# Performance work log

Measured on AMD Instinct MI355X. Metric: run time of the kernel, lower is better.

Reference implementation:

```python
import jax, jax.numpy as jnp
import numpy as np

B, L, HID, NH = 1, 2048, 3072, 24
HD = HID // NH          # 128
MLP = HID * 4           # 12288


def _layernorm(x, eps=1e-6):
    # LayerNorm without affine (pre_norm)
    mu = jnp.mean(x, axis=-1, keepdims=True)
    var = jnp.mean(jnp.square(x - mu), axis=-1, keepdims=True)
    return (x - mu) * jax.lax.rsqrt(var + eps)


def _rmsnorm(x, w):
    # torch.nn.RMSNorm with eps=None -> finfo(dtype).eps
    eps = jnp.finfo(x.dtype).eps
    ms = jnp.mean(jnp.square(x), axis=-1, keepdims=True)
    return x * jax.lax.rsqrt(ms + eps) * w


def _apply_rope(x, pe):
    # x: (B, L, H, D); pe: (B, 1, L, D//2, 2, 2)
    b, l, h, d = x.shape
    x_ = x.astype(jnp.float32).reshape(b, l, h, d // 2, 1, 2)
    f = pe[:, :, :, None]                       # (B,1,L,1,D//2,2,2)
    out = f[..., 0] * x_[..., 0] + f[..., 1] * x_[..., 1]
    return out.reshape(b, l, h, d).astype(x.dtype)


def setup_inputs() -> dict:
    key = jax.random.key(0)
    ks = jax.random.split(key, 16)
    s = 0.02
    # pe as proper 2x2 rotation matrices (EmbedND output structure)
    theta = jax.random.uniform(ks[0], (L, HD // 2), minval=0.0, maxval=2.0 * np.pi)
    cos, sin = jnp.cos(theta), jnp.sin(theta)
    rot = jnp.stack([jnp.stack([cos, -sin], -1), jnp.stack([sin, cos], -1)], -2)
    pe = rot[None, None].astype(jnp.float32)    # (1,1,L,HD//2,2,2)
    rnd = lambda k, shp: jax.random.normal(k, shp, jnp.float32)
    return {
        "x": rnd(ks[1], (B, L, HID)),
        "vec": rnd(ks[2], (B, HID)),
        "pe": pe,
        "w_mod": rnd(ks[3], (HID, 3 * HID)) * s,
        "b_mod": rnd(ks[4], (3 * HID,)) * s,
        "w_qkv": rnd(ks[5], (HID, 3 * HID)) * s,
        "b_qkv": rnd(ks[6], (3 * HID,)) * s,
        "w_fc1": rnd(ks[7], (HID, MLP)) * s,
        "b_fc1": rnd(ks[8], (MLP,)) * s,
        "w_fc2": rnd(ks[9], (MLP, HID)) * s,
        "b_fc2": rnd(ks[10], (HID,)) * s,
        "w_out": rnd(ks[11], (HID, HID)) * s,
        "b_out": rnd(ks[12], (HID,)) * s,
        "norm_q_w": jnp.ones((HD,), jnp.float32),
        "norm_k_w": jnp.ones((HD,), jnp.float32),
    }


def reference(x, vec, pe, w_mod, b_mod, w_qkv, b_qkv, w_fc1, b_fc1,
              w_fc2, b_fc2, w_out, b_out, norm_q_w, norm_k_w):
    # modulation: AWQ linear on silu(vec)
    mod = jax.nn.silu(vec) @ w_mod + b_mod            # (B, 3*HID)
    shift, scale, gate = jnp.split(mod[:, None, :], 3, axis=-1)
    x_mod = _layernorm(x) * (1.0 + scale) + shift      # (B, L, HID)

    # qkv projection (SVDQ linear, dequantized math == dense GEMM)
    qkv = x_mod @ w_qkv + b_qkv
    q, k, v = jnp.split(qkv, 3, axis=-1)
    q = _rmsnorm(q.reshape(B, L, NH, HD), norm_q_w)
    k = _rmsnorm(k.reshape(B, L, NH, HD), norm_k_w)
    q = _apply_rope(q, pe)
    k = _apply_rope(k, pe)
    v = v.reshape(B, L, NH, HD)

    # scaled dot-product attention
    scores = jnp.einsum("blhd,bmhd->bhlm", q, k) / jnp.sqrt(jnp.float32(HD))
    probs = jax.nn.softmax(scores, axis=-1)
    attn = jnp.einsum("bhlm,bmhd->blhd", probs, v).reshape(B, L, HID)

    # parallel MLP branch
    mlp = jax.nn.gelu(x_mod @ w_fc1 + b_fc1, approximate=True)
    mlp = mlp @ w_fc2 + b_fc2

    out = attn @ w_out + b_out + mlp
    return x + gate * out
```

## Files before the change

### kernel.cpp

```cpp
#include <hip/hip_runtime.h>
#include <hip/hip_bf16.h>
#include <stdint.h>


typedef __bf16 bf16;
typedef bf16 bf16x2 __attribute__((ext_vector_type(2)));
typedef bf16 bf16x4 __attribute__((ext_vector_type(4)));
typedef bf16 bf16x8 __attribute__((ext_vector_type(8)));
typedef float f32x4 __attribute__((ext_vector_type(4)));

#define L_SEQ 2048
#define HIDD  3072
#define NHH   24
#define HDD   128
#define MLPD  12288
#define N3Q   9216

__device__ __forceinline__ void gload_lds16(const bf16* g, bf16* l) {
  __builtin_amdgcn_global_load_lds(
      (const __attribute__((address_space(1))) unsigned int*)g,
      (__attribute__((address_space(3))) unsigned int*)l, 16, 0, 0);
}

__device__ __forceinline__ float gelu_tanh(float x) {
  float z = 0.7978845608028654f * (x + 0.044715f * x * x * x);
  float t = 1.f - 2.f / (__expf(2.f * z) + 1.f);
  return 0.5f * x * (1.f + t);
}

__global__ __launch_bounds__(256) void mod_partial(
    const float* __restrict__ vec, const float* __restrict__ w_mod,
    float* __restrict__ part) {
  __shared__ float sv[256];
  int y = blockIdx.y;
  int i0 = y * 256;
  {
    float xv = vec[i0 + threadIdx.x];
    sv[threadIdx.x] = xv / (1.f + __expf(-xv));
  }
  __syncthreads();
  int j = blockIdx.x * 256 + threadIdx.x;
  float acc = 0.f;
#pragma unroll 8
  for (int i = 0; i < 256; ++i)
    acc += sv[i] * w_mod[(size_t)(i0 + i) * N3Q + j];
  part[y * N3Q + j] = acc;
}

__global__ __launch_bounds__(256) void mod_reduce(
    const float* __restrict__ part, const float* __restrict__ b_mod,
    float* __restrict__ mod) {
  int j = blockIdx.x * 256 + threadIdx.x;
  float s = b_mod[j];
#pragma unroll
  for (int p = 0; p < 12; ++p) s += part[p * N3Q + j];
  mod[j] = s;
}

__global__ __launch_bounds__(256) void ln_mod_k(
    const float* __restrict__ x, const float* __restrict__ mod,
    bf16* __restrict__ xm) {
  __shared__ float sb[4];
  int l = blockIdx.x, t = threadIdx.x;
  const float* xr = x + (size_t)l * HIDD;
  float4 v[3];
  float s = 0.f;
#pragma unroll
  for (int p = 0; p < 3; ++p) {
    v[p] = *(const float4*)(xr + p * 1024 + t * 4);
    s += v[p].x + v[p].y + v[p].z + v[p].w;
  }
#pragma unroll
  for (int o = 32; o >= 1; o >>= 1) s += __shfl_xor(s, o);
  if (!(t & 63)) sb[t >> 6] = s;
  __syncthreads();
  float mean = (sb[0] + sb[1] + sb[2] + sb[3]) * (1.f / HIDD);
  __syncthreads();
  float vs = 0.f;
#pragma unroll
  for (int p = 0; p < 3; ++p) {
    float a = v[p].x - mean, b = v[p].y - mean, c = v[p].z - mean,
          d = v[p].w - mean;
    vs += a * a + b * b + c * c + d * d;
  }
#pragma unroll
  for (int o = 32; o >= 1; o >>= 1) vs += __shfl_xor(vs, o);
  if (!(t & 63)) sb[t >> 6] = vs;
  __syncthreads();
  float var = (sb[0] + sb[1] + sb[2] + sb[3]) * (1.f / HIDD);
  float rs = rsqrtf(var + 1e-6f);
#pragma unroll
  for (int p = 0; p < 3; ++p) {
    int j = p * 1024 + t * 4;
    float4 sc = *(const float4*)(mod + HIDD + j);
    float4 sh = *(const float4*)(mod + j);
    bf16x4 o;
    o[0] = (bf16)((v[p].x - mean) * rs * (1.f + sc.x) + sh.x);
    o[1] = (bf16)((v[p].y - mean) * rs * (1.f + sc.y) + sh.y);
    o[2] = (bf16)((v[p].z - mean) * rs * (1.f + sc.z) + sh.z);
    o[3] = (bf16)((v[p].w - mean) * rs * (1.f + sc.w) + sh.w);
    *(bf16x4*)(xm + (size_t)l * HIDD + j) = o;
  }
}

__global__ __launch_bounds__(256) void convT(
    const float* __restrict__ src, bf16* __restrict__ dst, int K, int N) {
  __shared__ bf16 tl[64 * 72];
  int n0 = blockIdx.x * 64, k0 = blockIdx.y * 64;
  int t = threadIdx.x;
#pragma unroll
  for (int p = 0; p < 4; ++p) {
    int idx = p * 256 + t;
    int kr = idx >> 4, c4 = (idx & 15) << 2;
    float4 v = *(const float4*)(src + (size_t)(k0 + kr) * N + n0 + c4);
    bf16x4 b;
    b[0] = (bf16)v.x; b[1] = (bf16)v.y; b[2] = (bf16)v.z; b[3] = (bf16)v.w;
    *(bf16x4*)(tl + kr * 72 + c4) = b;
  }
  __syncthreads();
#pragma unroll
  for (int p = 0; p < 2; ++p) {
    int idx = p * 256 + t;
    int nr = idx >> 3, c = idx & 7;
    bf16x8 o;
#pragma unroll
    for (int j = 0; j < 8; ++j) o[j] = tl[(c * 8 + j) * 72 + nr];
    *(bf16x8*)(dst + (size_t)(n0 + nr) * K + k0 + c * 8) = o;
  }
}

template <int EPI>
__global__ __launch_bounds__(256) void gemm_bt(
    const bf16* __restrict__ A, const bf16* __restrict__ BT,
    const float* __restrict__ bias, int lda, int klen,
    float* __restrict__ e_p0, float* __restrict__ e_p1,
    bf16* __restrict__ o0, bf16* __restrict__ o1, bf16* __restrict__ o2) {
  __shared__ bf16 As[2][128 * 64];
  __shared__ bf16 Bs[2][128 * 64];
  const int tid = threadIdx.x;
  const int lane = tid & 63, w = tid >> 6;
  const int wm = w >> 1, wn = w & 1;
  const int g = lane >> 4, r16 = lane & 15;
  const int row0 = blockIdx.x * 128, col0 = blockIdx.y * 128;
  const int kb = (EPI == 4) ? blockIdx.z * klen : 0;

  const int s_rr = tid >> 3, s_cc = tid & 7;
  const bf16* gA = A + (size_t)(row0 + s_rr) * lda + kb + ((s_cc ^ (s_rr & 7)) << 3);
  const bf16* gB = BT + (size_t)(col0 + s_rr) * lda + kb + ((s_cc ^ (s_rr & 7)) << 3);

  f32x4 acc[4][4] = {};

#define STAGE(buf, koff)                                                      \
  {                                                                           \
    _Pragma("unroll") for (int p = 0; p < 4; ++p) {                           \
      gload_lds16(gA + (size_t)(p * 32) * lda + (koff),                       \
                  &As[buf][(p * 4 + w) << 9]);                                \
      gload_lds16(gB + (size_t)(p * 32) * lda + (koff),                       \
                  &Bs[buf][(p * 4 + w) << 9]);                                \
    }                                                                         \
  }

  const int nk = klen >> 6;
  STAGE(0, 0);
  asm volatile("s_waitcnt vmcnt(0)" ::: "memory");
  __builtin_amdgcn_s_barrier();
  __builtin_amdgcn_sched_barrier(0);

  int cur = 0;
  for (int it = 0; it < nk; ++it) {
    if (it + 1 < nk) STAGE(cur ^ 1, (it + 1) * 64);
    const bf16* as = As[cur];
    const bf16* bs = Bs[cur];
#pragma unroll
    for (int kk = 0; kk < 2; ++kk) {
      bf16x8 af[4], bff[4];
#pragma unroll
      for (int m = 0; m < 4; ++m) {
        int rr = wm * 64 + m * 16 + r16;
        af[m] = *(const bf16x8*)(as + rr * 64 + (((kk * 4 + g) ^ (rr & 7)) << 3));
      }
#pragma unroll
      for (int n = 0; n < 4; ++n) {
        int rr = wn * 64 + n * 16 + r16;
        bff[n] = *(const bf16x8*)(bs + rr * 64 + (((kk * 4 + g) ^ (rr & 7)) << 3));
      }
#pragma unroll
      for (int m = 0; m < 4; ++m)
#pragma unroll
        for (int n = 0; n < 4; ++n)
          acc[m][n] = __builtin_amdgcn_mfma_f32_16x16x32_bf16(
              af[m], bff[n], acc[m][n], 0, 0, 0);
    }
    __builtin_amdgcn_sched_barrier(0);
    asm volatile("s_waitcnt vmcnt(0)" ::: "memory");
    __builtin_amdgcn_s_barrier();
    __builtin_amdgcn_sched_barrier(0);
    cur ^= 1;
  }
#undef STAGE

  float* psel = (EPI == 4) ? (blockIdx.z ? e_p1 : e_p0) : e_p0;
#pragma unroll
  for (int m = 0; m < 4; ++m) {
    int row = row0 + wm * 64 + m * 16 + g * 4;
#pragma unroll
    for (int n = 0; n < 4; ++n) {
      int col = col0 + wn * 64 + n * 16 + r16;
      float bv = (EPI == 4) ? 0.f : bias[col];
#pragma unroll
      for (int r = 0; r < 4; ++r) {
        float v = acc[m][n][r] + bv;
        if (EPI == 0) {
          bf16* dst;
          int cl = col;
          if (col < 3072) { dst = o0; }
          else if (col < 6144) { dst = o1; cl -= 3072; }
          else { dst = o2; cl -= 6144; }
          dst[(size_t)(row + r) * HIDD + cl] = (bf16)v;
        } else if (EPI == 1) {
          o0[(size_t)(row + r) * MLPD + col] = (bf16)gelu_tanh(v);
        } else {
          psel[(size_t)(row + r) * HIDD + col] = v;
        }
      }
    }
  }
}

__global__ __launch_bounds__(256) void final_k(
    const float* __restrict__ x, const float* __restrict__ tmp,
    const float* __restrict__ p0, const float* __restrict__ p1,
    const float* __restrict__ mod, const float* __restrict__ b_fc2,
    float* __restrict__ out) {
  int l = blockIdx.x, t = threadIdx.x;
#pragma unroll
  for (int p = 0; p < 3; ++p) {
    int c = p * 1024 + t * 4;
    size_t idx = (size_t)l * HIDD + c;
    float4 xv = *(const float4*)(x + idx);
    float4 tv = *(const float4*)(tmp + idx);
    float4 a0 = *(const float4*)(p0 + idx);
    float4 a1 = *(const float4*)(p1 + idx);
    float4 gv = *(const float4*)(mod + 2 * HIDD + c);
    float4 bv = *(const float4*)(b_fc2 + c);
    float4 o;
    o.x = xv.x + gv.x * (tv.x + a0.x + a1.x + bv.x);
    o.y = xv.y + gv.y * (tv.y + a0.y + a1.y + bv.y);
    o.z = xv.z + gv.z * (tv.z + a0.z + a1.z + bv.z);
    o.w = xv.w + gv.w * (tv.w + a0.w + a1.w + bv.w);
    *(float4*)(out + idx) = o;
  }
}

__global__ __launch_bounds__(256) void qknorm_rope_k(
    bf16* __restrict__ q, bf16* __restrict__ k, const float* __restrict__ pe,
    const float* __restrict__ qw, const float* __restrict__ kw) {
  int t = threadIdx.x, lane = t & 63, w = t >> 6;
  int pair = blockIdx.x * 4 + w;
  int h = pair % NHH, l = pair / NHH;
  size_t base = (size_t)l * HIDD + h * HDD + 2 * lane;
  float4 f = *(const float4*)(pe + (size_t)l * 256 + lane * 4);
  float2 wq = *(const float2*)(qw + 2 * lane);
  float2 wk = *(const float2*)(kw + 2 * lane);
  {
    bf16x2 xv = *(bf16x2*)(q + base);
    float x0 = (float)xv[0], x1 = (float)xv[1];
    float ss = x0 * x0 + x1 * x1;
#pragma unroll
    for (int o = 32; o >= 1; o >>= 1) ss += __shfl_xor(ss, o);
    float rs = rsqrtf(ss * (1.f / HDD) + 1.1920929e-7f);
    x0 *= rs * wq.x; x1 *= rs * wq.y;
    const float qs = 0.08838834764831845f;
    bf16x2 ov;
    ov[0] = (bf16)((f.x * x0 + f.y * x1) * qs);
    ov[1] = (bf16)((f.z * x0 + f.w * x1) * qs);
    *(bf16x2*)(q + base) = ov;
  }
  {
    bf16x2 xv = *(bf16x2*)(k + base);
    float x0 = (float)xv[0], x1 = (float)xv[1];
    float ss = x0 * x0 + x1 * x1;
#pragma unroll
    for (int o = 32; o >= 1; o >>= 1) ss += __shfl_xor(ss, o);
    float rs = rsqrtf(ss * (1.f / HDD) + 1.1920929e-7f);
    x0 *= rs * wk.x; x1 *= rs * wk.y;
    bf16x2 ov;
    ov[0] = (bf16)(f.x * x0 + f.y * x1);
    ov[1] = (bf16)(f.z * x0 + f.w * x1);
    *(bf16x2*)(k + base) = ov;
  }
}

__global__ __launch_bounds__(256) void vtrans_k(
    const bf16* __restrict__ v, bf16* __restrict__ vt) {
  __shared__ bf16 tl[128 * 128];
  int t = threadIdx.x, lt = blockIdx.x, h = blockIdx.y;
#pragma unroll
  for (int p = 0; p < 8; ++p) {
    int idx = p * 256 + t;
    int i = idx >> 4, c = idx & 15;
    bf16x8 val =
        *(const bf16x8*)(v + (size_t)(lt * 128 + i) * HIDD + h * HDD + c * 8);
    *(bf16x8*)(tl + i * 128 + ((c ^ (i & 15)) << 3)) = val;
  }
  __syncthreads();
#pragma unroll
  for (int p = 0; p < 8; ++p) {
    int idx = p * 256 + t;
    int j = idx >> 4, i8 = (idx & 15) << 3;
    bf16x8 o;
#pragma unroll
    for (int e = 0; e < 8; ++e) {
      int row = i8 + e;
      o[e] = tl[row * 128 + ((((j >> 3) ^ (row & 15)) << 3) | (j & 7))];
    }
    *(bf16x8*)(vt + ((size_t)h * HDD + j) * L_SEQ + lt * 128 + i8) = o;
  }
}

__global__ __launch_bounds__(256) void attn_k(
    const bf16* __restrict__ q, const bf16* __restrict__ k,
    const bf16* __restrict__ vt, bf16* __restrict__ out) {
  __shared__ bf16 Ks[64 * 128];
  __shared__ bf16 Vs[128 * 64];
  __shared__ bf16 Ps[4][16 * 72];
  int tid = threadIdx.x, lane = tid & 63, w = tid >> 6;
  int g = lane >> 4, r16 = lane & 15;
  int qt = blockIdx.x, h = blockIdx.y;
  int qbase = qt * 64 + w * 16;

  bf16x8 qreg[4];
  const bf16* qrow = q + (size_t)(qbase + r16) * HIDD + h * HDD;
#pragma unroll
  for (int c = 0; c < 4; ++c) qreg[c] = *(const bf16x8*)(qrow + c * 32 + g * 8);

  f32x4 acc[8] = {};
  float m_run = -3.0e38f, l_run = 0.f;
  bf16* ps = &Ps[w][0];

  for (int kv0 = 0; kv0 < L_SEQ; kv0 += 64) {
    __syncthreads();
#pragma unroll
    for (int p = 0; p < 4; ++p) {
      int ci = p * 256 + tid;
      {
        int rr = ci >> 4, cc = ci & 15;
        gload_lds16(k + (size_t)(kv0 + rr) * HIDD + h * HDD +
                        ((cc ^ (rr & 15)) << 3),
                    Ks + ((p * 4 + w) << 9));
      }
      {
        int rr = ci >> 3, cc = ci & 7;
        gload_lds16(vt + ((size_t)h * HDD + rr) * L_SEQ + kv0 +
                        ((cc ^ (rr & 7)) << 3),
                    Vs + ((p * 4 + w) << 9));
      }
    }
    __syncthreads();

    f32x4 st[4] = {};
#pragma unroll
    for (int m4 = 0; m4 < 4; ++m4) {
#pragma unroll
      for (int c = 0; c < 4; ++c) {
        int rr = m4 * 16 + r16;
        bf16x8 kf =
            *(const bf16x8*)(Ks + rr * 128 + (((c * 4 + g) ^ (rr & 15)) << 3));
        st[m4] =
            __builtin_amdgcn_mfma_f32_16x16x32_bf16(kf, qreg[c], st[m4], 0, 0, 0);
      }
    }
    float cmax = -3.0e38f;
#pragma unroll
    for (int m4 = 0; m4 < 4; ++m4)
#pragma unroll
      for (int r = 0; r < 4; ++r) cmax = fmaxf(cmax, st[m4][r]);
    cmax = fmaxf(cmax, __shfl_xor(cmax, 16));
    cmax = fmaxf(cmax, __shfl_xor(cmax, 32));
    float m_new = fmaxf(m_run, cmax);
    float corr = __expf(m_run - m_new);
    float psum = 0.f;
#pragma unroll
    for (int m4 = 0; m4 < 4; ++m4) {
      bf16x4 pk;
#pragma unroll
      for (int r = 0; r < 4; ++r) {
        float pv = __expf(st[m4][r] - m_new);
        psum += pv;
        pk[r] = (bf16)pv;
      }
      *(bf16x4*)(ps + r16 * 72 + m4 * 16 + g * 4) = pk;
    }
    psum += __shfl_xor(psum, 16);
    psum += __shfl_xor(psum, 32);
    l_run = l_run * corr + psum;
    m_run = m_new;
    float corr_r[4];
#pragma unroll
    for (int r = 0; r < 4; ++r) corr_r[r] = __shfl(corr, g * 4 + r);
#pragma unroll
    for (int nt = 0; nt < 8; ++nt)
#pragma unroll
      for (int r = 0; r < 4; ++r) acc[nt][r] *= corr_r[r];
#pragma unroll
    for (int ks = 0; ks < 2; ++ks) {
      bf16x8 pf = *(const bf16x8*)(ps + r16 * 72 + ks * 32 + g * 8);
#pragma unroll
      for (int nt = 0; nt < 8; ++nt) {
        int rr = nt * 16 + r16;
        bf16x8 vf =
            *(const bf16x8*)(Vs + rr * 64 + (((ks * 4 + g) ^ (rr & 7)) << 3));
        acc[nt] = __builtin_amdgcn_mfma_f32_16x16x32_bf16(pf, vf, acc[nt], 0, 0, 0);
      }
    }
  }
  float inv = 1.f / l_run;
  float inv_r[4];
#pragma unroll
  for (int r = 0; r < 4; ++r) inv_r[r] = __shfl(inv, g * 4 + r);
#pragma unroll
  for (int nt = 0; nt < 8; ++nt)
#pragma unroll
    for (int r = 0; r < 4; ++r)
      out[(size_t)(qbase + g * 4 + r) * HIDD + h * HDD + nt * 16 + r16] =
          (bf16)(acc[nt][r] * inv_r[r]);
}

extern "C" void kernel_launch(void* const* d_in, const int* in_sizes, int n_in,
                              void* d_out, int out_size, void* d_ws,
                              size_t ws_size, hipStream_t stream) {
  const float* x     = (const float*)d_in[0];
  const float* vec   = (const float*)d_in[1];
  const float* pe    = (const float*)d_in[2];
  const float* w_mod = (const float*)d_in[3];
  const float* b_mod = (const float*)d_in[4];
  const float* w_qkv = (const float*)d_in[5];
  const float* b_qkv = (const float*)d_in[6];
  const float* w_fc1 = (const float*)d_in[7];
  const float* b_fc1 = (const float*)d_in[8];
  const float* w_fc2 = (const float*)d_in[9];
  const float* b_fc2 = (const float*)d_in[10];
  const float* w_out = (const float*)d_in[11];
  const float* b_out = (const float*)d_in[12];
  const float* qw    = (const float*)d_in[13];
  const float* kw    = (const float*)d_in[14];
  float* out = (float*)d_out;

  char* ws = (char*)d_ws;
  float* mod  = (float*)(ws + 0);
  bf16* xmod  = (bf16*)(ws + 36864);
  bf16* qb    = (bf16*)(ws + 12619776);
  bf16* kb    = (bf16*)(ws + 25202688);
  bf16* vb    = (bf16*)(ws + 37785600);
  bf16* vt    = (bf16*)(ws + 50368512);
  bf16* att   = (bf16*)(ws + 62951424);
  bf16* mlp   = (bf16*)(ws + 75534336);
  float* tmp  = (float*)(ws + 125865984);
  bf16* wt    = (bf16*)(ws + 151031808);
  float* part = (float*)(ws + 125865984);
  float* pC   = (float*)(ws + 12619776);
  float* pD   = (float*)(ws + 37785600);

  mod_partial<<<dim3(36, 12), 256, 0, stream>>>(vec, w_mod, part);
  mod_reduce<<<36, 256, 0, stream>>>(part, b_mod, mod);
  ln_mod_k<<<2048, 256, 0, stream>>>(x, mod, xmod);

  convT<<<dim3(144, 48), 256, 0, stream>>>(w_qkv, wt, 3072, 9216);
  gemm_bt<0><<<dim3(16, 72), 256, 0, stream>>>(xmod, wt, b_qkv, 3072, 3072,
                                               nullptr, nullptr, qb, kb, vb);

  qknorm_rope_k<<<12288, 256, 0, stream>>>(qb, kb, pe, qw, kw);
  vtrans_k<<<dim3(16, 24), 256, 0, stream>>>(vb, vt);
  attn_k<<<dim3(32, 24), 256, 0, stream>>>(qb, kb, vt, att);

  convT<<<dim3(48, 48), 256, 0, stream>>>(w_out, wt, 3072, 3072);
  gemm_bt<2><<<dim3(16, 24), 256, 0, stream>>>(att, wt, b_out, 3072, 3072,
                                               tmp, nullptr, nullptr, nullptr,
                                               nullptr);

  convT<<<dim3(192, 48), 256, 0, stream>>>(w_fc1, wt, 3072, 12288);
  gemm_bt<1><<<dim3(16, 96), 256, 0, stream>>>(xmod, wt, b_fc1, 3072, 3072,
                                               nullptr, nullptr, mlp, nullptr,
                                               nullptr);

  convT<<<dim3(48, 192), 256, 0, stream>>>(w_fc2, wt, 12288, 3072);
  gemm_bt<4><<<dim3(16, 24, 2), 256, 0, stream>>>(mlp, wt, nullptr, 12288,
                                                  6144, pC, pD, nullptr,
                                                  nullptr, nullptr);
  final_k<<<2048, 256, 0, stream>>>(x, tmp, pC, pD, mod, b_fc2, out);
}
```

Baseline: 925.4 us.

## Replace 128x128 GEMM with 256x256 8-wave pipelined GEMM and split-K bf16 partials

```diff
diff --git a/kernel.cpp b/kernel.cpp
--- a/kernel.cpp
+++ b/kernel.cpp
@@ -15,6 +15,8 @@
 #define HDD   128
 #define MLPD  12288
 #define N3Q   9216
+
+struct PB { bf16* p[8]; };
 
 __device__ __forceinline__ void gload_lds16(const bf16* g, bf16* l) {
   __builtin_amdgcn_global_load_lds(
@@ -130,141 +132,154 @@
 }
 
 template <int EPI>
-__global__ __launch_bounds__(256) void gemm_bt(
+__global__ __launch_bounds__(512, 2) void gemm256(
     const bf16* __restrict__ A, const bf16* __restrict__ BT,
-    const float* __restrict__ bias, int lda, int klen,
-    float* __restrict__ e_p0, float* __restrict__ e_p1,
-    bf16* __restrict__ o0, bf16* __restrict__ o1, bf16* __restrict__ o2) {
-  __shared__ bf16 As[2][128 * 64];
-  __shared__ bf16 Bs[2][128 * 64];
+    const float* __restrict__ bias, int lda, int klen, int ldc, PB dst,
+    bf16* __restrict__ o1) {
+  __shared__ bf16 LA[2][2][8192];
+  __shared__ bf16 LB[2][2][8192];
   const int tid = threadIdx.x;
-  const int lane = tid & 63, w = tid >> 6;
-  const int wm = w >> 1, wn = w & 1;
+  const int w = tid >> 6, lane = tid & 63;
+  const int wm = w >> 2, wn = w & 3;
   const int g = lane >> 4, r16 = lane & 15;
-  const int row0 = blockIdx.x * 128, col0 = blockIdx.y * 128;
-  const int kb = (EPI == 4) ? blockIdx.z * klen : 0;
-
-  const int s_rr = tid >> 3, s_cc = tid & 7;
-  const bf16* gA = A + (size_t)(row0 + s_rr) * lda + kb + ((s_cc ^ (s_rr & 7)) << 3);
-  const bf16* gB = BT + (size_t)(col0 + s_rr) * lda + kb + ((s_cc ^ (s_rr & 7)) << 3);
-
-  f32x4 acc[4][4] = {};
-
-#define STAGE(buf, koff)                                                      \
-  {                                                                           \
-    _Pragma("unroll") for (int p = 0; p < 4; ++p) {                           \
-      gload_lds16(gA + (size_t)(p * 32) * lda + (koff),                       \
-                  &As[buf][(p * 4 + w) << 9]);                                \
-      gload_lds16(gB + (size_t)(p * 32) * lda + (koff),                       \
-                  &Bs[buf][(p * 4 + w) << 9]);                                \
-    }                                                                         \
-  }
-
+  const int row0 = blockIdx.x * 256, col0 = blockIdx.y * 256;
+  const size_t kb = (size_t)blockIdx.z * klen;
+
+  const int s_r = tid >> 3, s_c = tid & 7;
+  const bf16* gA = A + (size_t)(row0 + s_r) * lda + kb + ((s_c ^ (s_r & 7)) << 3);
+  const bf16* gB = BT + (size_t)(col0 + s_r) * lda + kb + ((s_c ^ (s_r & 7)) << 3);
+  const int wofs = w * 512;
+
+#define STG_A(buf, h, t)                                                       \
+  do {                                                                         \
+    gload_lds16(gA + (size_t)((h) * 128) * lda + (t) * 64, &LA[buf][h][wofs]); \
+    gload_lds16(gA + (size_t)((h) * 128 + 64) * lda + (t) * 64,                \
+                &LA[buf][h][4096 + wofs]);                                     \
+  } while (0)
+#define STG_B(buf, h, t)                                                       \
+  do {                                                                         \
+    gload_lds16(gB + (size_t)((h) * 128) * lda + (t) * 64, &LB[buf][h][wofs]); \
+    gload_lds16(gB + (size_t)((h) * 128 + 64) * lda + (t) * 64,                \
+                &LB[buf][h][4096 + wofs]);                                     \
+  } while (0)
+#define LGKM0()                                               \
+  do {                                                        \
+    asm volatile("s_waitcnt lgkmcnt(0)" ::: "memory");        \
+    __builtin_amdgcn_sched_barrier(0);                        \
+  } while (0)
+#define MF(mb, AF, BF)                                                     \
+  do {                                                                     \
+    __builtin_amdgcn_s_setprio(1);                                         \
+    _Pragma("unroll") for (int m_ = 0; m_ < 4; ++m_)                       \
+        _Pragma("unroll") for (int n_ = 0; n_ < 4; ++n_)                   \
+            acc[(mb) + m_][n_] = __builtin_amdgcn_mfma_f32_16x16x32_bf16(  \
+                AF[(mb) + m_], BF[n_], acc[(mb) + m_][n_], 0, 0, 0);       \
+    __builtin_amdgcn_s_setprio(0);                                         \
+  } while (0)
+
+  f32x4 acc[8][4] = {};
   const int nk = klen >> 6;
-  STAGE(0, 0);
-  asm volatile("s_waitcnt vmcnt(0)" ::: "memory");
+  const int swz0 = (g ^ (r16 & 7)) << 3;
+  const int swz1 = ((4 + g) ^ (r16 & 7)) << 3;
+  const int brow = (wn & 1) * 64;
+  const int hb = wn >> 1;
+
+  STG_A(0, 0, 0); STG_A(0, 1, 0); STG_B(0, 0, 0); STG_B(0, 1, 0);
+  STG_B(1, 0, 1); STG_A(1, 0, 1); STG_A(1, 1, 1);
+  asm volatile("s_waitcnt vmcnt(6)" ::: "memory");
   __builtin_amdgcn_s_barrier();
-  __builtin_amdgcn_sched_barrier(0);
-
-  int cur = 0;
-  for (int it = 0; it < nk; ++it) {
-    if (it + 1 < nk) STAGE(cur ^ 1, (it + 1) * 64);
-    const bf16* as = As[cur];
-    const bf16* bs = Bs[cur];
-#pragma unroll
-    for (int kk = 0; kk < 2; ++kk) {
-      bf16x8 af[4], bff[4];
-#pragma unroll
-      for (int m = 0; m < 4; ++m) {
-        int rr = wm * 64 + m * 16 + r16;
-        af[m] = *(const bf16x8*)(as + rr * 64 + (((kk * 4 + g) ^ (rr & 7)) << 3));
-      }
-#pragma unroll
-      for (int n = 0; n < 4; ++n) {
-        int rr = wn * 64 + n * 16 + r16;
-        bff[n] = *(const bf16x8*)(bs + rr * 64 + (((kk * 4 + g) ^ (rr & 7)) << 3));
-      }
-#pragma unroll
-      for (int m = 0; m < 4; ++m)
-#pragma unroll
-        for (int n = 0; n < 4; ++n)
-          acc[m][n] = __builtin_amdgcn_mfma_f32_16x16x32_bf16(
-              af[m], bff[n], acc[m][n], 0, 0, 0);
-    }
-    __builtin_amdgcn_sched_barrier(0);
-    asm volatile("s_waitcnt vmcnt(0)" ::: "memory");
-    __builtin_amdgcn_s_barrier();
-    __builtin_amdgcn_sched_barrier(0);
-    cur ^= 1;
-  }
-#undef STAGE
-
-  float* psel = (EPI == 4) ? (blockIdx.z ? e_p1 : e_p0) : e_p0;
-#pragma unroll
-  for (int m = 0; m < 4; ++m) {
-    int row = row0 + wm * 64 + m * 16 + g * 4;
+
+  for (int t = 0; t < nk; ++t) {
+    const int buf = t & 1;
+    const bf16* la = LA[buf][wm];
+    const bf16* lb = LB[buf][hb];
+    bf16x8 af0[8], af1[8], bf0[4], bf1[4];
+
+#pragma unroll
+    for (int m = 0; m < 8; ++m)
+      af0[m] = *(const bf16x8*)(la + (m * 16 + r16) * 64 + swz0);
+#pragma unroll
+    for (int n = 0; n < 4; ++n)
+      bf0[n] = *(const bf16x8*)(lb + (brow + n * 16 + r16) * 64 + swz0);
+    __builtin_amdgcn_s_barrier();
+    LGKM0();
+    if (t + 1 < nk) STG_B(buf ^ 1, 1, t + 1);
+    MF(0, af0, bf0);
+    __builtin_amdgcn_s_barrier();
+
+#pragma unroll
+    for (int n = 0; n < 4; ++n)
+      bf1[n] = *(const bf16x8*)(lb + (brow + n * 16 + r16) * 64 + swz1);
+    __builtin_amdgcn_s_barrier();
+    LGKM0();
+    if (t + 2 < nk) STG_B(buf, 0, t + 2);
+    MF(4, af0, bf0);
+    __builtin_amdgcn_s_barrier();
+
+#pragma unroll
+    for (int m = 0; m < 4; ++m)
+      af1[m] = *(const bf16x8*)(la + (m * 16 + r16) * 64 + swz1);
+    __builtin_amdgcn_s_barrier();
+    LGKM0();
+    MF(0, af1, bf1);
+    __builtin_amdgcn_s_barrier();
+
+#pragma unroll
+    for (int m = 4; m < 8; ++m)
+      af1[m] = *(const bf16x8*)(la + (m * 16 + r16) * 64 + swz1);
+    __builtin_amdgcn_s_barrier();
+    LGKM0();
+    if (t + 2 < nk) { STG_A(buf, 0, t + 2); STG_A(buf, 1, t + 2); }
+    if (t < nk - 2) {
+      asm volatile("s_waitcnt vmcnt(6)" ::: "memory");
+    } else if (t == nk - 2) {
+      asm volatile("s_waitcnt vmcnt(0)" ::: "memory");
+    }
+    MF(4, af1, bf1);
+    __builtin_amdgcn_s_barrier();
+  }
+#undef STG_A
+#undef STG_B
+#undef LGKM0
+#undef MF
+
+  bf16* dp = (EPI == 0) ? dst.p[blockIdx.z] : o1;
+#pragma unroll
+  for (int m = 0; m < 8; ++m) {
+    int row = row0 + wm * 128 + m * 16 + g * 4;
 #pragma unroll
     for (int n = 0; n < 4; ++n) {
       int col = col0 + wn * 64 + n * 16 + r16;
-      float bv = (EPI == 4) ? 0.f : bias[col];
+      float bv = (EPI == 1) ? bias[col] : 0.f;
 #pragma unroll
       for (int r = 0; r < 4; ++r) {
         float v = acc[m][n][r] + bv;
-        if (EPI == 0) {
-          bf16* dst;
-          int cl = col;
-          if (col < 3072) { dst = o0; }
-          else if (col < 6144) { dst = o1; cl -= 3072; }
-          else { dst = o2; cl -= 6144; }
-          dst[(size_t)(row + r) * HIDD + cl] = (bf16)v;
-        } else if (EPI == 1) {
-          o0[(size_t)(row + r) * MLPD + col] = (bf16)gelu_tanh(v);
-        } else {
-          psel[(size_t)(row + r) * HIDD + col] = v;
-        }
+        if (EPI == 1) v = gelu_tanh(v);
+        dp[(size_t)(row + r) * ldc + col] = (bf16)v;
       }
     }
   }
 }
 
-__global__ __launch_bounds__(256) void final_k(
-    const float* __restrict__ x, const float* __restrict__ tmp,
-    const float* __restrict__ p0, const float* __restrict__ p1,
-    const float* __restrict__ mod, const float* __restrict__ b_fc2,
-    float* __restrict__ out) {
-  int l = blockIdx.x, t = threadIdx.x;
-#pragma unroll
-  for (int p = 0; p < 3; ++p) {
-    int c = p * 1024 + t * 4;
-    size_t idx = (size_t)l * HIDD + c;
-    float4 xv = *(const float4*)(x + idx);
-    float4 tv = *(const float4*)(tmp + idx);
-    float4 a0 = *(const float4*)(p0 + idx);
-    float4 a1 = *(const float4*)(p1 + idx);
-    float4 gv = *(const float4*)(mod + 2 * HIDD + c);
-    float4 bv = *(const float4*)(b_fc2 + c);
-    float4 o;
-    o.x = xv.x + gv.x * (tv.x + a0.x + a1.x + bv.x);
-    o.y = xv.y + gv.y * (tv.y + a0.y + a1.y + bv.y);
-    o.z = xv.z + gv.z * (tv.z + a0.z + a1.z + bv.z);
-    o.w = xv.w + gv.w * (tv.w + a0.w + a1.w + bv.w);
-    *(float4*)(out + idx) = o;
-  }
-}
-
 __global__ __launch_bounds__(256) void qknorm_rope_k(
-    bf16* __restrict__ q, bf16* __restrict__ k, const float* __restrict__ pe,
-    const float* __restrict__ qw, const float* __restrict__ kw) {
+    const bf16* __restrict__ P0, const bf16* __restrict__ P1,
+    const float* __restrict__ b_qkv, const float* __restrict__ pe,
+    const float* __restrict__ qw, const float* __restrict__ kw,
+    bf16* __restrict__ qb, bf16* __restrict__ kb) {
   int t = threadIdx.x, lane = t & 63, w = t >> 6;
   int pair = blockIdx.x * 4 + w;
   int h = pair % NHH, l = pair / NHH;
-  size_t base = (size_t)l * HIDD + h * HDD + 2 * lane;
+  size_t qi = (size_t)l * N3Q + h * HDD + 2 * lane;
+  size_t ob = (size_t)l * HIDD + h * HDD + 2 * lane;
   float4 f = *(const float4*)(pe + (size_t)l * 256 + lane * 4);
   float2 wq = *(const float2*)(qw + 2 * lane);
   float2 wk = *(const float2*)(kw + 2 * lane);
   {
-    bf16x2 xv = *(bf16x2*)(q + base);
-    float x0 = (float)xv[0], x1 = (float)xv[1];
+    bf16x2 a = *(const bf16x2*)(P0 + qi);
+    bf16x2 b = *(const bf16x2*)(P1 + qi);
+    float2 bq = *(const float2*)(b_qkv + h * HDD + 2 * lane);
+    float x0 = (float)a[0] + (float)b[0] + bq.x;
+    float x1 = (float)a[1] + (float)b[1] + bq.y;
     float ss = x0 * x0 + x1 * x1;
 #pragma unroll
     for (int o = 32; o >= 1; o >>= 1) ss += __shfl_xor(ss, o);
@@ -274,11 +289,14 @@
     bf16x2 ov;
     ov[0] = (bf16)((f.x * x0 + f.y * x1) * qs);
     ov[1] = (bf16)((f.z * x0 + f.w * x1) * qs);
-    *(bf16x2*)(q + base) = ov;
+    *(bf16x2*)(qb + ob) = ov;
   }
   {
-    bf16x2 xv = *(bf16x2*)(k + base);
-    float x0 = (float)xv[0], x1 = (float)xv[1];
+    bf16x2 a = *(const bf16x2*)(P0 + qi + HIDD);
+    bf16x2 b = *(const bf16x2*)(P1 + qi + HIDD);
+    float2 bk = *(const float2*)(b_qkv + HIDD + h * HDD + 2 * lane);
+    float x0 = (float)a[0] + (float)b[0] + bk.x;
+    float x1 = (float)a[1] + (float)b[1] + bk.y;
     float ss = x0 * x0 + x1 * x1;
 #pragma unroll
     for (int o = 32; o >= 1; o >>= 1) ss += __shfl_xor(ss, o);
@@ -287,20 +305,27 @@
     bf16x2 ov;
     ov[0] = (bf16)(f.x * x0 + f.y * x1);
     ov[1] = (bf16)(f.z * x0 + f.w * x1);
-    *(bf16x2*)(k + base) = ov;
+    *(bf16x2*)(kb + ob) = ov;
   }
 }
 
 __global__ __launch_bounds__(256) void vtrans_k(
-    const bf16* __restrict__ v, bf16* __restrict__ vt) {
+    const bf16* __restrict__ P0, const bf16* __restrict__ P1,
+    const float* __restrict__ b_qkv, bf16* __restrict__ vt) {
   __shared__ bf16 tl[128 * 128];
   int t = threadIdx.x, lt = blockIdx.x, h = blockIdx.y;
 #pragma unroll
   for (int p = 0; p < 8; ++p) {
     int idx = p * 256 + t;
     int i = idx >> 4, c = idx & 15;
-    bf16x8 val =
-        *(const bf16x8*)(v + (size_t)(lt * 128 + i) * HIDD + h * HDD + c * 8);
+    size_t gi = (size_t)(lt * 128 + i) * N3Q + 2 * HIDD + h * HDD + c * 8;
+    bf16x8 a = *(const bf16x8*)(P0 + gi);
+    bf16x8 b = *(const bf16x8*)(P1 + gi);
+    bf16x8 val;
+#pragma unroll
+    for (int e = 0; e < 8; ++e)
+      val[e] = (bf16)((float)a[e] + (float)b[e] +
+                      b_qkv[2 * HIDD + h * HDD + c * 8 + e]);
     *(bf16x8*)(tl + i * 128 + ((c ^ (i & 15)) << 3)) = val;
   }
   __syncthreads();
@@ -424,6 +449,51 @@
     for (int r = 0; r < 4; ++r)
       out[(size_t)(qbase + g * 4 + r) * HIDD + h * HDD + nt * 16 + r16] =
           (bf16)(acc[nt][r] * inv_r[r]);
+}
+
+__global__ __launch_bounds__(256) void osum_k(
+    const bf16* __restrict__ a, const bf16* __restrict__ b,
+    float* __restrict__ o) {
+  size_t i = ((size_t)blockIdx.x * 256 + threadIdx.x) * 4;
+  bf16x4 va = *(const bf16x4*)(a + i);
+  bf16x4 vb = *(const bf16x4*)(b + i);
+  float4 s;
+  s.x = (float)va[0] + (float)vb[0];
+  s.y = (float)va[1] + (float)vb[1];
+  s.z = (float)va[2] + (float)vb[2];
+  s.w = (float)va[3] + (float)vb[3];
+  *(float4*)(o + i) = s;
+}
+
+__global__ __launch_bounds__(256) void final_k(
+    const float* __restrict__ x, PB ps, const float* __restrict__ mod,
+    const float* __restrict__ b_out, const float* __restrict__ b_fc2,
+    float* __restrict__ out) {
+  int l = blockIdx.x, t = threadIdx.x;
+#pragma unroll
+  for (int p = 0; p < 3; ++p) {
+    int c = p * 1024 + t * 4;
+    size_t idx = (size_t)l * HIDD + c;
+    float4 xv = *(const float4*)(x + idx);
+    float4 gv = *(const float4*)(mod + 2 * HIDD + c);
+    float4 bo = *(const float4*)(b_out + c);
+    float4 bf = *(const float4*)(b_fc2 + c);
+    float4 da = *(const float4*)(out + idx);
+    float a0 = da.x + bo.x + bf.x, a1 = da.y + bo.y + bf.y;
+    float a2 = da.z + bo.z + bf.z, a3 = da.w + bo.w + bf.w;
+#pragma unroll
+    for (int i = 0; i < 8; ++i) {
+      bf16x4 v = *(const bf16x4*)(ps.p[i] + idx);
+      a0 += (float)v[0]; a1 += (float)v[1];
+      a2 += (float)v[2]; a3 += (float)v[3];
+    }
+    float4 o;
+    o.x = xv.x + gv.x * a0;
+    o.y = xv.y + gv.y * a1;
+    o.z = xv.z + gv.z * a2;
+    o.w = xv.w + gv.w * a3;
+    *(float4*)(out + idx) = o;
+  }
 }
 
 extern "C" void kernel_launch(void* const* d_in, const int* in_sizes, int n_in,
@@ -450,42 +520,54 @@
   float* mod  = (float*)(ws + 0);
   bf16* xmod  = (bf16*)(ws + 36864);
   bf16* qb    = (bf16*)(ws + 12619776);
-  bf16* kb    = (bf16*)(ws + 25202688);
-  bf16* vb    = (bf16*)(ws + 37785600);
-  bf16* vt    = (bf16*)(ws + 50368512);
-  bf16* att   = (bf16*)(ws + 62951424);
-  bf16* mlp   = (bf16*)(ws + 75534336);
-  float* tmp  = (float*)(ws + 125865984);
-  bf16* wt    = (bf16*)(ws + 151031808);
-  float* part = (float*)(ws + 125865984);
-  float* pC   = (float*)(ws + 12619776);
-  float* pD   = (float*)(ws + 37785600);
+  bf16* kbuf  = (bf16*)(ws + 25202688);
+  bf16* vt    = (bf16*)(ws + 37785600);
+  bf16* att   = (bf16*)(ws + 50368512);
+  bf16* mlp   = (bf16*)(ws + 62951424);
+  bf16* wt    = (bf16*)(ws + 113283072);
+  bf16* P0    = (bf16*)(ws + 188780544);
+  bf16* P1    = (bf16*)(ws + 62951424);
+  float* part = (float*)(ws + 188780544);
+  bf16* pO0   = qb;
+  bf16* pO1   = kbuf;
+  bf16* pF0   = xmod;
+  bf16* pF1   = vt;
+  bf16* pF2   = att;
+  bf16* pF3   = (bf16*)(ws + 188780544);
+  bf16* pF4   = (bf16*)(ws + 201363456);
+  bf16* pF5   = (bf16*)(ws + 213946368);
+  bf16* pF6   = qb;
+  bf16* pF7   = kbuf;
 
   mod_partial<<<dim3(36, 12), 256, 0, stream>>>(vec, w_mod, part);
   mod_reduce<<<36, 256, 0, stream>>>(part, b_mod, mod);
   ln_mod_k<<<2048, 256, 0, stream>>>(x, mod, xmod);
 
   convT<<<dim3(144, 48), 256, 0, stream>>>(w_qkv, wt, 3072, 9216);
-  gemm_bt<0><<<dim3(16, 72), 256, 0, stream>>>(xmod, wt, b_qkv, 3072, 3072,
-                                               nullptr, nullptr, qb, kb, vb);
-
-  qknorm_rope_k<<<12288, 256, 0, stream>>>(qb, kb, pe, qw, kw);
-  vtrans_k<<<dim3(16, 24), 256, 0, stream>>>(vb, vt);
-  attn_k<<<dim3(32, 24), 256, 0, stream>>>(qb, kb, vt, att);
+  PB Pq = {}; Pq.p[0] = P0; Pq.p[1] = P1;
+  gemm256<0><<<dim3(8, 36, 2), 512, 0, stream>>>(xmod, wt, nullptr, 3072, 1536,
+                                                 9216, Pq, nullptr);
+  qknorm_rope_k<<<12288, 256, 0, stream>>>(P0, P1, b_qkv, pe, qw, kw, qb, kbuf);
+  vtrans_k<<<dim3(16, 24), 256, 0, stream>>>(P0, P1, b_qkv, vt);
+  attn_k<<<dim3(32, 24), 256, 0, stream>>>(qb, kbuf, vt, att);
 
   convT<<<dim3(48, 48), 256, 0, stream>>>(w_out, wt, 3072, 3072);
-  gemm_bt<2><<<dim3(16, 24), 256, 0, stream>>>(att, wt, b_out, 3072, 3072,
-                                               tmp, nullptr, nullptr, nullptr,
-                                               nullptr);
+  PB Po = {}; Po.p[0] = pO0; Po.p[1] = pO1;
+  gemm256<0><<<dim3(8, 12, 2), 512, 0, stream>>>(att, wt, nullptr, 3072, 1536,
+                                                 3072, Po, nullptr);
+  osum_k<<<6144, 256, 0, stream>>>(pO0, pO1, out);
 
   convT<<<dim3(192, 48), 256, 0, stream>>>(w_fc1, wt, 3072, 12288);
-  gemm_bt<1><<<dim3(16, 96), 256, 0, stream>>>(xmod, wt, b_fc1, 3072, 3072,
-                                               nullptr, nullptr, mlp, nullptr,
-                                               nullptr);
+  PB Pz = {};
+  gemm256<1><<<dim3(8, 48, 1), 512, 0, stream>>>(xmod, wt, b_fc1, 3072, 3072,
+                                                 12288, Pz, mlp);
 
   convT<<<dim3(48, 192), 256, 0, stream>>>(w_fc2, wt, 12288, 3072);
-  gemm_bt<4><<<dim3(16, 24, 2), 256, 0, stream>>>(mlp, wt, nullptr, 12288,
-                                                  6144, pC, pD, nullptr,
-                                                  nullptr, nullptr);
-  final_k<<<2048, 256, 0, stream>>>(x, tmp, pC, pD, mod, b_fc2, out);
-}
+  PB Pf = {};
+  Pf.p[0] = pF0; Pf.p[1] = pF1; Pf.p[2] = pF2; Pf.p[3] = pF3;
+  Pf.p[4] = pF4; Pf.p[5] = pF5; Pf.p[6] = pF6; Pf.p[7] = pF7;
+  gemm256<0><<<dim3(8, 12, 8), 512, 0, stream>>>(mlp, wt, nullptr, 12288, 1536,
+                                                 3072, Pf, nullptr);
+
+  final_k<<<2048, 256, 0, stream>>>(x, Pf, mod, b_out, b_fc2, out);
+}
```

New measurement: 972.7 us. +5.1%, slower.
